# Kernel optimization log

Hardware: AMD Instinct MI355X
Metric: run time of the kernel (lower is better)

The kernel has to match this reference:

```python
import jax, jax.numpy as jnp
import numpy as np

N, C, H, W = 4, 256, 64, 64
K, G, PAD, STRIDE, DIL = 3, 8, 1, 1, 1
GC = C // G      # channels per group
P = K * K        # sampling points per group
HIN, WIN = H + 2 * PAD, W + 2 * PAD
BN_EPS = 1e-5
LN_EPS = 1e-5


def setup_inputs():
    key = jax.random.key(0)
    ks = jax.random.split(key, 8)
    f32 = jnp.float32
    return {
        "x": jax.random.normal(ks[0], (N, C, H, W), dtype=f32),
        "w_in": jax.random.normal(ks[1], (C, C), dtype=f32) * 0.05,
        "b_in": jnp.zeros((C,), f32),
        "w_dw": jax.random.normal(ks[2], (C, 1, K, K), dtype=f32) * 0.1,
        "b_dw": jnp.zeros((C,), f32),
        "ln_g": jnp.ones((C,), f32), "ln_b": jnp.zeros((C,), f32),
        "w_off": jax.random.normal(ks[3], (C, G * P * 2), dtype=f32) * 0.01,
        "b_off": jax.random.normal(ks[4], (G * P * 2,), dtype=f32) * 0.01,
        "w_mask": jax.random.normal(ks[5], (C, G * P), dtype=f32) * 0.01,
        "b_mask": jnp.zeros((G * P,), f32),
        "w_out": jax.random.normal(ks[6], (C, C), dtype=f32) * 0.05,
        "b_out": jnp.zeros((C,), f32),
        "bn_g": jnp.ones((C,), f32), "bn_b": jnp.zeros((C,), f32),
        "bn_mean": jnp.zeros((C,), f32), "bn_var": jnp.ones((C,), f32),
    }


def _bilinear(img, grid):
    # img: (B, Cc, Hh, Ww); grid: (B, S, P, 2) normalized to [-1,1],
    # matches F.grid_sample(mode='bilinear', padding_mode='zeros', align_corners=False)
    B, Cc, Hh, Ww = img.shape
    gx = (grid[..., 0] + 1.0) * 0.5 * Ww - 0.5
    gy = (grid[..., 1] + 1.0) * 0.5 * Hh - 0.5
    x0 = jnp.floor(gx)
    y0 = jnp.floor(gy)
    wx = gx - x0
    wy = gy - y0
    flat = img.reshape(B, Cc, Hh * Ww)

    def tap(xi, yi, wgt):
        valid = (xi >= 0) & (xi <= Ww - 1) & (yi >= 0) & (yi <= Hh - 1)
        idx = (jnp.clip(yi, 0, Hh - 1) * Ww + jnp.clip(xi, 0, Ww - 1)).astype(jnp.int32)
        v = jax.vmap(lambda im, ix: im[:, ix])(flat, idx)   # (B, Cc, S, P)
        return v * (wgt * valid.astype(img.dtype))[:, None]

    return (tap(x0, y0, (1 - wx) * (1 - wy)) + tap(x0 + 1, y0, wx * (1 - wy))
            + tap(x0, y0 + 1, (1 - wx) * wy) + tap(x0 + 1, y0 + 1, wx * wy))


def _forward(x, w_in, b_in, w_dw, b_dw, ln_g, ln_b, w_off, b_off,
             w_mask, b_mask, w_out, b_out, bn_g, bn_b, bn_mean, bn_var):
    xl = jnp.transpose(x, (0, 2, 3, 1))                      # (N,H,W,C) channels-last
    x_proj = xl @ w_in + b_in                                # input_proj
    # depthwise conv + LayerNorm + GELU feature branch for offset/mask prediction
    dw = jax.lax.conv_general_dilated(
        x, w_dw, (1, 1), ((PAD, PAD), (PAD, PAD)),
        feature_group_count=C, dimension_numbers=("NCHW", "OIHW", "NCHW"))
    dw = jnp.transpose(dw + b_dw[None, :, None, None], (0, 2, 3, 1))
    mu = dw.mean(-1, keepdims=True)
    var = ((dw - mu) ** 2).mean(-1, keepdims=True)
    dw = (dw - mu) * jax.lax.rsqrt(var + LN_EPS) * ln_g + ln_b
    x1 = jax.nn.gelu(dw, approximate=False)
    offset = x1 @ w_off + b_off                              # (N,H,W,G*P*2)
    mask = jax.nn.softmax((x1 @ w_mask + b_mask).reshape(N, H, W, G, P), axis=-1)
    # reference points + dilation kernel grid, normalized to padded input, (x,y) order
    ry = ((DIL * (K - 1)) // 2 + 0.5 + jnp.arange(H, dtype=x.dtype) * STRIDE) / HIN
    rx = ((DIL * (K - 1)) // 2 + 0.5 + jnp.arange(W, dtype=x.dtype) * STRIDE) / WIN
    ref = jnp.stack(jnp.broadcast_arrays(rx[None, :], ry[:, None]), axis=-1)  # (H,W,2)
    px = (jnp.arange(K, dtype=x.dtype) * DIL - (DIL * (K - 1)) // 2) / WIN
    py = (jnp.arange(K, dtype=x.dtype) * DIL - (DIL * (K - 1)) // 2) / HIN
    gx, gy = jnp.meshgrid(px, py, indexing="ij")             # kw-major flattening as in DCNv3
    kgrid = jnp.stack([gx, gy], -1).reshape(P, 2)
    norm = jnp.array([WIN, HIN], dtype=x.dtype)
    loc = (ref[None, :, :, None, None, :] + kgrid[None, None, None, None, :, :]
           + offset.reshape(N, H, W, G, P, 2) / norm)        # (N,H,W,G,P,2), offset_scale=1
    sgrid = 2.0 * loc - 1.0
    # group-split padded value tensor and deformable sampling
    xp = jnp.pad(x_proj, ((0, 0), (PAD, PAD), (PAD, PAD), (0, 0)))
    img = jnp.transpose(xp, (0, 3, 1, 2)).reshape(N * G, GC, HIN, WIN)
    sg = jnp.transpose(sgrid.reshape(N, H * W, G, P, 2), (0, 2, 1, 3, 4)).reshape(N * G, H * W, P, 2)
    sampled = _bilinear(img, sg)                             # (N*G, GC, H*W, P)
    m = jnp.transpose(mask.reshape(N, H * W, G, P), (0, 2, 1, 3)).reshape(N * G, 1, H * W, P)
    agg = (sampled * m).sum(-1)                              # (N*G, GC, H*W)
    y = jnp.transpose(agg.reshape(N, C, H * W), (0, 2, 1)).reshape(N, H, W, C)
    y = y @ w_out + b_out                                    # output_proj
    y = jnp.transpose(y, (0, 3, 1, 2))                       # back to NCHW
    y = (y - bn_mean[None, :, None, None]) * jax.lax.rsqrt(bn_var + BN_EPS)[None, :, None, None]
    y = y * bn_g[None, :, None, None] + bn_b[None, :, None, None]
    return y * jax.nn.sigmoid(y)                             # SiLU (Conv.default_act)


def reference(x, w_in, b_in, w_dw, b_dw, ln_g, ln_b, w_off, b_off,
              w_mask, b_mask, w_out, b_out, bn_g, bn_b, bn_mean, bn_var):
    return _forward(x, w_in, b_in, w_dw, b_dw, ln_g, ln_b, w_off, b_off,
                    w_mask, b_mask, w_out, b_out, bn_g, bn_b, bn_mean, bn_var)
```

## Files before the change

### kernel.cpp

```cpp
#include <hip/hip_runtime.h>
#include <math.h>

#define NB   4
#define CCH  256
#define HH   64
#define WW   64
#define GG   8
#define GCH  32
#define PP   9
#define HIN  66
#define WIN  66
#define HWSZ 4096
#define NPIX 16384

#define XP_ELEMS  (NB*HIN*WIN*CCH)
#define X1_ELEMS  (NPIX*CCH)
#define AGG_ELEMS (NPIX*CCH)
#define OFF_ELEMS (NPIX*144)
#define MSK_ELEMS (NPIX*72)

typedef __attribute__((ext_vector_type(8))) short bf16x8;
typedef __attribute__((ext_vector_type(4))) float f32x4;

__device__ __forceinline__ unsigned short f2bf(float f) {
    unsigned int u = __float_as_uint(f);
    unsigned int r = (u + 0x7FFFu + ((u >> 16) & 1u)) >> 16;
    return (unsigned short)r;
}
__device__ __forceinline__ float bf2f(unsigned short s) {
    return __uint_as_float(((unsigned int)s) << 16);
}
__device__ __forceinline__ unsigned int f2bf_pk(float lo, float hi) {
    return (unsigned int)f2bf(lo) | ((unsigned int)f2bf(hi) << 16);
}

#define AK 40

__global__ __launch_bounds__(64) void k_zero_ring(unsigned short* __restrict__ xp)
{
    int b = blockIdx.x;
    int n = b / 260;
    int rp = b % 260;
    int h, w;
    if (rp < 66)       { h = 0;        w = rp; }
    else if (rp < 132) { h = 65;       w = rp - 66; }
    else if (rp < 196) { h = rp - 131; w = 0; }
    else               { h = rp - 195; w = 65; }
    uint2 z = make_uint2(0u, 0u);
    *(uint2*)&xp[(((size_t)n * HIN + h) * WIN + w) * CCH + threadIdx.x * 4] = z;
}

__global__ __launch_bounds__(256) void k_gemm_in(
    const float* __restrict__ x, const float* __restrict__ w_in,
    const float* __restrict__ b_in, unsigned short* __restrict__ xp)
{
    __shared__ short As[128 * AK];
    __shared__ short Ws[64 * AK];

    const int m0  = blockIdx.x * 128;
    const int co0 = blockIdx.y * 64;
    const int tid = threadIdx.x;
    const int n   = m0 >> 12;
    const int hw0 = m0 & 4095;

    const int wave = tid >> 6;
    const int lane = tid & 63;
    const int r16  = lane & 15;
    const int quad = lane >> 4;
    const int mw   = wave * 32;

    const float* xa = x + (size_t)n * CCH * HWSZ + hw0;

    f32x4 acc[2][4];
#pragma unroll
    for (int i = 0; i < 2; i++)
#pragma unroll
        for (int j = 0; j < 4; j++) acc[i][j] = (f32x4){0.f, 0.f, 0.f, 0.f};

    for (int k0 = 0; k0 < CCH; k0 += 32) {
#pragma unroll
        for (int l = 0; l < 8; l++) {
            int idx = tid + l * 256;
            int m = idx & 127, kp = idx >> 7;
            float v0 = xa[(size_t)(k0 + 2 * kp) * HWSZ + m];
            float v1 = xa[(size_t)(k0 + 2 * kp + 1) * HWSZ + m];
            ((unsigned int*)As)[(m * AK) / 2 + kp] = f2bf_pk(v0, v1);
        }
#pragma unroll
        for (int l = 0; l < 4; l++) {
            int idx = tid + l * 256;
            int nn = idx & 63, kp = idx >> 6;
            float v0 = w_in[(size_t)(k0 + 2 * kp) * CCH + co0 + nn];
            float v1 = w_in[(size_t)(k0 + 2 * kp + 1) * CCH + co0 + nn];
            ((unsigned int*)Ws)[(nn * AK) / 2 + kp] = f2bf_pk(v0, v1);
        }
        __syncthreads();

        bf16x8 a0 = *(const bf16x8*)&As[(mw + r16) * AK + quad * 8];
        bf16x8 a1 = *(const bf16x8*)&As[(mw + 16 + r16) * AK + quad * 8];
#pragma unroll
        for (int nt = 0; nt < 4; nt++) {
            bf16x8 bfr = *(const bf16x8*)&Ws[(nt * 16 + r16) * AK + quad * 8];
            acc[0][nt] = __builtin_amdgcn_mfma_f32_16x16x32_bf16(a0, bfr, acc[0][nt], 0, 0, 0);
            acc[1][nt] = __builtin_amdgcn_mfma_f32_16x16x32_bf16(a1, bfr, acc[1][nt], 0, 0, 0);
        }
        __syncthreads();
    }

#pragma unroll
    for (int nt = 0; nt < 4; nt++) {
        int co = co0 + nt * 16 + r16;
        float bias = b_in[co];
#pragma unroll
        for (int mt = 0; mt < 2; mt++) {
            int mbase = mw + mt * 16 + quad * 4;
#pragma unroll
            for (int r = 0; r < 4; r++) {
                int hw = hw0 + mbase + r;
                int h = hw >> 6, w = hw & 63;
                xp[(((size_t)n * HIN + (h + 1)) * WIN + (w + 1)) * CCH + co] =
                    f2bf(acc[mt][nt][r] + bias);
            }
        }
    }
}

#define SDW_STRIDE 258
__global__ __launch_bounds__(512) void k_dw_ln_gelu(
    const float* __restrict__ x, const float* __restrict__ w_dw,
    const float* __restrict__ b_dw, const float* __restrict__ ln_g,
    const float* __restrict__ ln_b, unsigned short* __restrict__ x1)
{
    __shared__ unsigned short sdw[64 * SDW_STRIDE];
    __shared__ float r1s[8][64];
    __shared__ float r2s[8][64];
    __shared__ float mu_s[64];
    __shared__ float rs_s[64];

    const int h = blockIdx.x;
    const int n = blockIdx.y;
    const int tid = threadIdx.x;
    const int wave = tid >> 6;
    const int lane = tid & 63;

    const float* xn = x + (size_t)n * CCH * HWSZ;
    const bool h0ok = (h > 0);
    const bool h2ok = (h < HH - 1);

    float s1 = 0.f, s2 = 0.f;

#pragma unroll 4
    for (int it = 0; it < 32; it++) {
        const int c = it * 8 + wave;
        const float* xc = xn + (size_t)c * HWSZ + h * WW + lane;
        float v0 = h0ok ? xc[-WW] : 0.f;
        float v1 = xc[0];
        float v2 = h2ok ? xc[WW] : 0.f;

        const float* wk = w_dw + c * 9;
        float acc = b_dw[c];

        float l0 = __shfl_up(v0, 1);  if (lane == 0)  l0 = 0.f;
        float r0 = __shfl_down(v0, 1); if (lane == 63) r0 = 0.f;
        acc += wk[0] * l0 + wk[1] * v0 + wk[2] * r0;

        float l1 = __shfl_up(v1, 1);  if (lane == 0)  l1 = 0.f;
        float r1 = __shfl_down(v1, 1); if (lane == 63) r1 = 0.f;
        acc += wk[3] * l1 + wk[4] * v1 + wk[5] * r1;

        float l2 = __shfl_up(v2, 1);  if (lane == 0)  l2 = 0.f;
        float r2 = __shfl_down(v2, 1); if (lane == 63) r2 = 0.f;
        acc += wk[6] * l2 + wk[7] * v2 + wk[8] * r2;

        s1 += acc;
        s2 += acc * acc;
        sdw[lane * SDW_STRIDE + c] = f2bf(acc);
    }

    r1s[wave][lane] = s1;
    r2s[wave][lane] = s2;
    __syncthreads();

    if (tid < 64) {
        float a1 = 0.f, a2 = 0.f;
#pragma unroll
        for (int q = 0; q < 8; q++) { a1 += r1s[q][tid]; a2 += r2s[q][tid]; }
        float mu = a1 * (1.0f / 256.0f);
        float var = a2 * (1.0f / 256.0f) - mu * mu;
        mu_s[tid] = mu;
        rs_s[tid] = rsqrtf(var + 1e-5f);
    }
    __syncthreads();

    const int c0 = (tid & 63) * 4;
    const int wq = tid >> 6;
    float g4[4], b4[4];
#pragma unroll
    for (int i = 0; i < 4; i++) { g4[i] = ln_g[c0 + i]; b4[i] = ln_b[c0 + i]; }

    unsigned short* x1p = x1 + (((size_t)n * HH + h) * WW) * CCH + c0;
#pragma unroll
    for (int pass = 0; pass < 8; pass++) {
        int w = wq + pass * 8;
        float mu = mu_s[w], rs = rs_s[w];
        const unsigned short* row = &sdw[w * SDW_STRIDE + c0];
        unsigned short tmp[4];
#pragma unroll
        for (int i = 0; i < 4; i++) {
            float v = (bf2f(row[i]) - mu) * rs * g4[i] + b4[i];
            tmp[i] = f2bf(0.5f * v * (1.0f + erff(v * 0.70710678118654752f)));
        }
        ushort4 o; o.x = tmp[0]; o.y = tmp[1]; o.z = tmp[2]; o.w = tmp[3];
        *(ushort4*)&x1p[(size_t)w * CCH] = o;
    }
}

__global__ __launch_bounds__(256) void k_gemm_offmask(
    const unsigned short* __restrict__ x1, const float* __restrict__ w_off,
    const float* __restrict__ b_off, const float* __restrict__ w_mask,
    const float* __restrict__ b_mask, float* __restrict__ off,
    float* __restrict__ msk)
{
    __shared__ short As[128 * AK];
    __shared__ short Ws[64 * AK];

    const int m0  = blockIdx.x * 128;
    const int co0 = blockIdx.y * 64;
    const int tid = threadIdx.x;

    const int wave = tid >> 6;
    const int lane = tid & 63;
    const int r16  = lane & 15;
    const int quad = lane >> 4;
    const int mw   = wave * 32;

    f32x4 acc[2][4];
#pragma unroll
    for (int i = 0; i < 2; i++)
#pragma unroll
        for (int j = 0; j < 4; j++) acc[i][j] = (f32x4){0.f, 0.f, 0.f, 0.f};

    for (int k0 = 0; k0 < CCH; k0 += 32) {
#pragma unroll
        for (int l = 0; l < 2; l++) {
            int idx = tid + l * 256;
            int m = idx >> 2, kq = idx & 3;
            uint4 v = *(const uint4*)&x1[(size_t)(m0 + m) * CCH + k0 + kq * 8];
            *(uint4*)&As[m * AK + kq * 8] = v;
        }
#pragma unroll
        for (int l = 0; l < 4; l++) {
            int idx = tid + l * 256;
            int nn = idx & 63, kp = idx >> 6;
            int col = co0 + nn;
            float v0 = 0.f, v1 = 0.f;
            if (col < 144) {
                v0 = w_off[(size_t)(k0 + 2 * kp) * 144 + col];
                v1 = w_off[(size_t)(k0 + 2 * kp + 1) * 144 + col];
            } else if (col < 216) {
                v0 = w_mask[(size_t)(k0 + 2 * kp) * 72 + col - 144];
                v1 = w_mask[(size_t)(k0 + 2 * kp + 1) * 72 + col - 144];
            }
            ((unsigned int*)Ws)[(nn * AK) / 2 + kp] = f2bf_pk(v0, v1);
        }
        __syncthreads();

        bf16x8 a0 = *(const bf16x8*)&As[(mw + r16) * AK + quad * 8];
        bf16x8 a1 = *(const bf16x8*)&As[(mw + 16 + r16) * AK + quad * 8];
#pragma unroll
        for (int nt = 0; nt < 4; nt++) {
            bf16x8 bfr = *(const bf16x8*)&Ws[(nt * 16 + r16) * AK + quad * 8];
            acc[0][nt] = __builtin_amdgcn_mfma_f32_16x16x32_bf16(a0, bfr, acc[0][nt], 0, 0, 0);
            acc[1][nt] = __builtin_amdgcn_mfma_f32_16x16x32_bf16(a1, bfr, acc[1][nt], 0, 0, 0);
        }
        __syncthreads();
    }

#pragma unroll
    for (int nt = 0; nt < 4; nt++) {
        int col = co0 + nt * 16 + r16;
        if (col >= 216) continue;
        float bias = (col < 144) ? b_off[col] : b_mask[col - 144];
#pragma unroll
        for (int mt = 0; mt < 2; mt++) {
            int mbase = m0 + mw + mt * 16 + quad * 4;
#pragma unroll
            for (int r = 0; r < 4; r++) {
                int p = mbase + r;
                float v = acc[mt][nt][r] + bias;
                if (col < 144) off[(size_t)p * 144 + col] = v;
                else           msk[(size_t)p * 72 + col - 144] = v;
            }
        }
    }
}

__global__ __launch_bounds__(256) void k_sample_agg(
    const unsigned short* __restrict__ xp, const float* __restrict__ off,
    const float* __restrict__ msk, unsigned short* __restrict__ agg)
{
    __shared__ float  sm[288];
    __shared__ int2   tco[288];
    __shared__ float4 twt[288];

    const int tid = threadIdx.x;
    const int s0 = blockIdx.x * 4;

    if (tid < 32) {
        const int pix = tid >> 3, g = tid & 7;
        const float* mskp = msk + (size_t)(s0 + pix) * 72 + g * 9;
        float e[9];
        float mx = -1e30f;
#pragma unroll
        for (int p = 0; p < PP; p++) { e[p] = mskp[p]; mx = fmaxf(mx, e[p]); }
        float sum = 0.f;
#pragma unroll
        for (int p = 0; p < PP; p++) { e[p] = __expf(e[p] - mx); sum += e[p]; }
        float rs = 1.0f / sum;
#pragma unroll
        for (int p = 0; p < PP; p++) sm[tid * 9 + p] = e[p] * rs;
    }
    __syncthreads();

    for (int idx = tid; idx < 288; idx += 256) {
        int pix = idx / 72;
        int rem = idx - pix * 72;
        int g = rem / 9;
        int p = rem - g * 9;
        int s = s0 + pix;
        int hw = s & 4095;
        int h = hw >> 6, w = hw & 63;
        const float* offp = off + (size_t)s * 144 + g * 18 + p * 2;
        float ox = offp[0], oy = offp[1];
        int i = p / 3, j = p - i * 3;
        float fx = (float)(w + i) + ox;
        float fy = (float)(h + j) + oy;
        float x0f = floorf(fx), y0f = floorf(fy);
        int x0 = (int)x0f, y0 = (int)y0f;
        float wx = fx - x0f, wy = fy - y0f;
        float m = sm[idx];
        float w00 = (1.f - wx) * (1.f - wy) * m;
        float w10 = wx * (1.f - wy) * m;
        float w01 = (1.f - wx) * wy * m;
        float w11 = wx * wy * m;
        int x1c = x0 + 1, y1c = y0 + 1;
        if (!((x0  >= 0) && (x0  < WIN))) { w00 = 0.f; w01 = 0.f; }
        if (!((x1c >= 0) && (x1c < WIN))) { w10 = 0.f; w11 = 0.f; }
        if (!((y0  >= 0) && (y0  < HIN))) { w00 = 0.f; w10 = 0.f; }
        if (!((y1c >= 0) && (y1c < HIN))) { w01 = 0.f; w11 = 0.f; }
        int cx0 = min(max(x0, 0), WIN - 1), cx1 = min(max(x1c, 0), WIN - 1);
        int cy0 = min(max(y0, 0), HIN - 1), cy1 = min(max(y1c, 0), HIN - 1);
        tco[idx] = make_int2(cx0 | (cx1 << 16), cy0 | (cy1 << 16));
        twt[idx] = make_float4(w00, w10, w01, w11);
    }
    __syncthreads();

    const int pix = tid >> 6;
    const int lane = tid & 63;
    const int g = lane >> 3, c4 = lane & 7;
    const int s = s0 + pix;
    const int n = s >> 12;
    const unsigned short* base = xp + (size_t)n * HIN * WIN * CCH + g * GCH + c4 * 4;
    const int tbase = pix * 72 + g * 9;

    float ax = 0.f, ay = 0.f, az = 0.f, aw = 0.f;
#pragma unroll
    for (int p = 0; p < PP; p++) {
        int2 cc = tco[tbase + p];
        float4 wt = twt[tbase + p];
        int cx0 = cc.x & 0xFFFF, cx1 = cc.x >> 16;
        int cy0 = cc.y & 0xFFFF, cy1 = cc.y >> 16;
        const unsigned short* r0 = base + (size_t)(cy0 * WIN) * CCH;
        const unsigned short* r1 = base + (size_t)(cy1 * WIN) * CCH;
        ushort4 v00 = *(const ushort4*)&r0[(size_t)cx0 * CCH];
        ushort4 v10 = *(const ushort4*)&r0[(size_t)cx1 * CCH];
        ushort4 v01 = *(const ushort4*)&r1[(size_t)cx0 * CCH];
        ushort4 v11 = *(const ushort4*)&r1[(size_t)cx1 * CCH];
        ax += wt.x * bf2f(v00.x) + wt.y * bf2f(v10.x) + wt.z * bf2f(v01.x) + wt.w * bf2f(v11.x);
        ay += wt.x * bf2f(v00.y) + wt.y * bf2f(v10.y) + wt.z * bf2f(v01.y) + wt.w * bf2f(v11.y);
        az += wt.x * bf2f(v00.z) + wt.y * bf2f(v10.z) + wt.z * bf2f(v01.z) + wt.w * bf2f(v11.z);
        aw += wt.x * bf2f(v00.w) + wt.y * bf2f(v10.w) + wt.z * bf2f(v01.w) + wt.w * bf2f(v11.w);
    }

    ushort4 o; o.x = f2bf(ax); o.y = f2bf(ay); o.z = f2bf(az); o.w = f2bf(aw);
    *(ushort4*)&agg[(size_t)s * CCH + g * GCH + c4 * 4] = o;
}

__global__ __launch_bounds__(256) void k_gemm_out(
    const unsigned short* __restrict__ agg, const float* __restrict__ w_out,
    const float* __restrict__ b_out, const float* __restrict__ bn_g,
    const float* __restrict__ bn_b, const float* __restrict__ bn_mean,
    const float* __restrict__ bn_var, float* __restrict__ out)
{
    __shared__ short As[128 * AK];
    __shared__ short Ws[64 * AK];

    const int m0  = blockIdx.x * 128;
    const int co0 = blockIdx.y * 64;
    const int tid = threadIdx.x;
    const int n   = m0 >> 12;
    const int hw0 = m0 & 4095;

    const int wave = tid >> 6;
    const int lane = tid & 63;
    const int r16  = lane & 15;
    const int quad = lane >> 4;
    const int mw   = wave * 32;

    f32x4 acc[2][4];
#pragma unroll
    for (int i = 0; i < 2; i++)
#pragma unroll
        for (int j = 0; j < 4; j++) acc[i][j] = (f32x4){0.f, 0.f, 0.f, 0.f};

    for (int k0 = 0; k0 < CCH; k0 += 32) {
#pragma unroll
        for (int l = 0; l < 2; l++) {
            int idx = tid + l * 256;
            int m = idx >> 2, kq = idx & 3;
            uint4 v = *(const uint4*)&agg[(size_t)(m0 + m) * CCH + k0 + kq * 8];
            *(uint4*)&As[m * AK + kq * 8] = v;
        }
#pragma unroll
        for (int l = 0; l < 4; l++) {
            int idx = tid + l * 256;
            int nn = idx & 63, kp = idx >> 6;
            float v0 = w_out[(size_t)(k0 + 2 * kp) * CCH + co0 + nn];
            float v1 = w_out[(size_t)(k0 + 2 * kp + 1) * CCH + co0 + nn];
            ((unsigned int*)Ws)[(nn * AK) / 2 + kp] = f2bf_pk(v0, v1);
        }
        __syncthreads();

        bf16x8 a0 = *(const bf16x8*)&As[(mw + r16) * AK + quad * 8];
        bf16x8 a1 = *(const bf16x8*)&As[(mw + 16 + r16) * AK + quad * 8];
#pragma unroll
        for (int nt = 0; nt < 4; nt++) {
            bf16x8 bfr = *(const bf16x8*)&Ws[(nt * 16 + r16) * AK + quad * 8];
            acc[0][nt] = __builtin_amdgcn_mfma_f32_16x16x32_bf16(a0, bfr, acc[0][nt], 0, 0, 0);
            acc[1][nt] = __builtin_amdgcn_mfma_f32_16x16x32_bf16(a1, bfr, acc[1][nt], 0, 0, 0);
        }
        __syncthreads();
    }

#pragma unroll
    for (int nt = 0; nt < 4; nt++) {
        int co = co0 + nt * 16 + r16;
        float mean = bn_mean[co];
        float rstd = rsqrtf(bn_var[co] + 1e-5f);
        float gg = bn_g[co], bb = bn_b[co], bo = b_out[co];
#pragma unroll
        for (int mt = 0; mt < 2; mt++) {
            int hwb = hw0 + mw + mt * 16 + quad * 4;
            float tmp[4];
#pragma unroll
            for (int r = 0; r < 4; r++) {
                float y = acc[mt][nt][r] + bo;
                float yh = (y - mean) * rstd * gg + bb;
                tmp[r] = yh / (1.0f + __expf(-yh));
            }
            float4 v = make_float4(tmp[0], tmp[1], tmp[2], tmp[3]);
            *(float4*)&out[((size_t)n * CCH + co) * HWSZ + hwb] = v;
        }
    }
}

extern "C" void kernel_launch(void* const* d_in, const int* in_sizes, int n_in,
                              void* d_out, int out_size, void* d_ws, size_t ws_size,
                              hipStream_t stream)
{
    const float* x       = (const float*)d_in[0];
    const float* w_in    = (const float*)d_in[1];
    const float* b_in    = (const float*)d_in[2];
    const float* w_dw    = (const float*)d_in[3];
    const float* b_dw    = (const float*)d_in[4];
    const float* ln_g    = (const float*)d_in[5];
    const float* ln_b    = (const float*)d_in[6];
    const float* w_off   = (const float*)d_in[7];
    const float* b_off   = (const float*)d_in[8];
    const float* w_mask  = (const float*)d_in[9];
    const float* b_mask  = (const float*)d_in[10];
    const float* w_out   = (const float*)d_in[11];
    const float* b_out   = (const float*)d_in[12];
    const float* bn_g    = (const float*)d_in[13];
    const float* bn_b    = (const float*)d_in[14];
    const float* bn_mean = (const float*)d_in[15];
    const float* bn_var  = (const float*)d_in[16];
    float* out = (float*)d_out;

    unsigned short* xp  = (unsigned short*)d_ws;
    unsigned short* x1  = xp + XP_ELEMS;
    unsigned short* agg = x1 + X1_ELEMS;
    float* off = (float*)(agg + AGG_ELEMS);
    float* msk = off + OFF_ELEMS;

    k_zero_ring<<<dim3(1040), 64, 0, stream>>>(xp);
    k_gemm_in<<<dim3(128, 4), 256, 0, stream>>>(x, w_in, b_in, xp);
    k_dw_ln_gelu<<<dim3(64, 4), 512, 0, stream>>>(x, w_dw, b_dw, ln_g, ln_b, x1);
    k_gemm_offmask<<<dim3(128, 4), 256, 0, stream>>>(x1, w_off, b_off, w_mask, b_mask, off, msk);
    k_sample_agg<<<dim3(4096), 256, 0, stream>>>(xp, off, msk, agg);
    k_gemm_out<<<dim3(128, 4), 256, 0, stream>>>(agg, w_out, b_out, bn_g, bn_b, bn_mean, bn_var, out);
}
```

Baseline: 181.5 us.

## Pre-convert input and weights to bf16 once; widen sampling loads to 8 channels

```diff
diff --git a/kernel.cpp b/kernel.cpp
--- a/kernel.cpp
+++ b/kernel.cpp
@@ -13,9 +13,13 @@
 #define HWSZ 4096
 #define NPIX 16384
 
+#define X16_ELEMS (NPIX*CCH)
 #define XP_ELEMS  (NB*HIN*WIN*CCH)
 #define X1_ELEMS  (NPIX*CCH)
 #define AGG_ELEMS (NPIX*CCH)
+#define WIN16_ELEMS (CCH*CCH)
+#define WOUT16_ELEMS (CCH*CCH)
+#define WOM16_ELEMS (CCH*216)
 #define OFF_ELEMS (NPIX*144)
 #define MSK_ELEMS (NPIX*72)
 
@@ -30,28 +34,58 @@
 __device__ __forceinline__ float bf2f(unsigned short s) {
     return __uint_as_float(((unsigned int)s) << 16);
 }
-__device__ __forceinline__ unsigned int f2bf_pk(float lo, float hi) {
-    return (unsigned int)f2bf(lo) | ((unsigned int)f2bf(hi) << 16);
-}
 
 #define AK 40
 
-__global__ __launch_bounds__(64) void k_zero_ring(unsigned short* __restrict__ xp)
-{
-    int b = blockIdx.x;
-    int n = b / 260;
-    int rp = b % 260;
-    int h, w;
-    if (rp < 66)       { h = 0;        w = rp; }
-    else if (rp < 132) { h = 65;       w = rp - 66; }
-    else if (rp < 196) { h = rp - 131; w = 0; }
-    else               { h = rp - 195; w = 65; }
-    uint2 z = make_uint2(0u, 0u);
-    *(uint2*)&xp[(((size_t)n * HIN + h) * WIN + w) * CCH + threadIdx.x * 4] = z;
+__global__ __launch_bounds__(256) void k_prep(
+    const float* __restrict__ x, const float* __restrict__ w_in,
+    const float* __restrict__ w_off, const float* __restrict__ w_mask,
+    const float* __restrict__ w_out, unsigned short* __restrict__ x16,
+    unsigned short* __restrict__ w_in16, unsigned short* __restrict__ wom16,
+    unsigned short* __restrict__ w_out16, unsigned short* __restrict__ xp)
+{
+    const int b = blockIdx.x;
+    const int tid = threadIdx.x;
+    if (b < 2048) {
+        size_t i0 = (size_t)b * 2048 + tid * 4;
+#pragma unroll
+        for (int h = 0; h < 2; h++) {
+            float4 v = *(const float4*)&x[i0 + h * 1024];
+            ushort4 o;
+            o.x = f2bf(v.x); o.y = f2bf(v.y); o.z = f2bf(v.z); o.w = f2bf(v.w);
+            *(ushort4*)&x16[i0 + h * 1024] = o;
+        }
+    } else if (b < 2096) {
+        int gtid = (b - 2048) * 256 + tid;
+        for (int i = gtid; i < 186368; i += 12288) {
+            if (i < 65536) {
+                w_in16[i] = f2bf(w_in[i]);
+            } else if (i < 131072) {
+                int j = i - 65536;
+                w_out16[j] = f2bf(w_out[j]);
+            } else {
+                int j = i - 131072;
+                int r = j / 216, c = j - r * 216;
+                float v = (c < 144) ? w_off[r * 144 + c] : w_mask[r * 72 + c - 144];
+                wom16[j] = f2bf(v);
+            }
+        }
+    } else {
+        int idx = (b - 2096) * 256 + tid;
+        int seg = idx >> 6, ln = idx & 63;
+        int n = seg / 260, rp = seg % 260;
+        int h, w;
+        if (rp < 66)       { h = 0;        w = rp; }
+        else if (rp < 132) { h = 65;       w = rp - 66; }
+        else if (rp < 196) { h = rp - 131; w = 0; }
+        else               { h = rp - 195; w = 65; }
+        uint2 z = make_uint2(0u, 0u);
+        *(uint2*)&xp[(((size_t)n * HIN + h) * WIN + w) * CCH + ln * 4] = z;
+    }
 }
 
 __global__ __launch_bounds__(256) void k_gemm_in(
-    const float* __restrict__ x, const float* __restrict__ w_in,
+    const unsigned short* __restrict__ x16, const unsigned short* __restrict__ w16,
     const float* __restrict__ b_in, unsigned short* __restrict__ xp)
 {
     __shared__ short As[128 * AK];
@@ -69,7 +103,7 @@
     const int quad = lane >> 4;
     const int mw   = wave * 32;
 
-    const float* xa = x + (size_t)n * CCH * HWSZ + hw0;
+    const unsigned short* xa = x16 + (size_t)n * CCH * HWSZ + hw0;
 
     f32x4 acc[2][4];
 #pragma unroll
@@ -78,21 +112,27 @@
         for (int j = 0; j < 4; j++) acc[i][j] = (f32x4){0.f, 0.f, 0.f, 0.f};
 
     for (int k0 = 0; k0 < CCH; k0 += 32) {
-#pragma unroll
-        for (int l = 0; l < 8; l++) {
-            int idx = tid + l * 256;
-            int m = idx & 127, kp = idx >> 7;
-            float v0 = xa[(size_t)(k0 + 2 * kp) * HWSZ + m];
-            float v1 = xa[(size_t)(k0 + 2 * kp + 1) * HWSZ + m];
-            ((unsigned int*)As)[(m * AK) / 2 + kp] = f2bf_pk(v0, v1);
-        }
 #pragma unroll
         for (int l = 0; l < 4; l++) {
             int idx = tid + l * 256;
-            int nn = idx & 63, kp = idx >> 6;
-            float v0 = w_in[(size_t)(k0 + 2 * kp) * CCH + co0 + nn];
-            float v1 = w_in[(size_t)(k0 + 2 * kp + 1) * CCH + co0 + nn];
-            ((unsigned int*)Ws)[(nn * AK) / 2 + kp] = f2bf_pk(v0, v1);
+            int m = idx & 127, kph = idx >> 7;
+            unsigned int u0 = xa[(size_t)(k0 + 4 * kph + 0) * HWSZ + m];
+            unsigned int u1 = xa[(size_t)(k0 + 4 * kph + 1) * HWSZ + m];
+            unsigned int u2 = xa[(size_t)(k0 + 4 * kph + 2) * HWSZ + m];
+            unsigned int u3 = xa[(size_t)(k0 + 4 * kph + 3) * HWSZ + m];
+            uint2 pk = make_uint2(u0 | (u1 << 16), u2 | (u3 << 16));
+            *(uint2*)&As[m * AK + kph * 4] = pk;
+        }
+#pragma unroll
+        for (int l = 0; l < 2; l++) {
+            int idx = tid + l * 256;
+            int nn = idx & 63, kph = idx >> 6;
+            unsigned int u0 = w16[(size_t)(k0 + 4 * kph + 0) * CCH + co0 + nn];
+            unsigned int u1 = w16[(size_t)(k0 + 4 * kph + 1) * CCH + co0 + nn];
+            unsigned int u2 = w16[(size_t)(k0 + 4 * kph + 2) * CCH + co0 + nn];
+            unsigned int u3 = w16[(size_t)(k0 + 4 * kph + 3) * CCH + co0 + nn];
+            uint2 pk = make_uint2(u0 | (u1 << 16), u2 | (u3 << 16));
+            *(uint2*)&Ws[nn * AK + kph * 4] = pk;
         }
         __syncthreads();
 
@@ -127,7 +167,7 @@
 
 #define SDW_STRIDE 258
 __global__ __launch_bounds__(512) void k_dw_ln_gelu(
-    const float* __restrict__ x, const float* __restrict__ w_dw,
+    const unsigned short* __restrict__ x16, const float* __restrict__ w_dw,
     const float* __restrict__ b_dw, const float* __restrict__ ln_g,
     const float* __restrict__ ln_b, unsigned short* __restrict__ x1)
 {
@@ -143,7 +183,7 @@
     const int wave = tid >> 6;
     const int lane = tid & 63;
 
-    const float* xn = x + (size_t)n * CCH * HWSZ;
+    const unsigned short* xn = x16 + (size_t)n * CCH * HWSZ;
     const bool h0ok = (h > 0);
     const bool h2ok = (h < HH - 1);
 
@@ -152,10 +192,10 @@
 #pragma unroll 4
     for (int it = 0; it < 32; it++) {
         const int c = it * 8 + wave;
-        const float* xc = xn + (size_t)c * HWSZ + h * WW + lane;
-        float v0 = h0ok ? xc[-WW] : 0.f;
-        float v1 = xc[0];
-        float v2 = h2ok ? xc[WW] : 0.f;
+        const unsigned short* xc = xn + (size_t)c * HWSZ + h * WW + lane;
+        float v0 = h0ok ? bf2f(xc[-WW]) : 0.f;
+        float v1 = bf2f(xc[0]);
+        float v2 = h2ok ? bf2f(xc[WW]) : 0.f;
 
         const float* wk = w_dw + c * 9;
         float acc = b_dw[c];
@@ -216,10 +256,9 @@
 }
 
 __global__ __launch_bounds__(256) void k_gemm_offmask(
-    const unsigned short* __restrict__ x1, const float* __restrict__ w_off,
-    const float* __restrict__ b_off, const float* __restrict__ w_mask,
-    const float* __restrict__ b_mask, float* __restrict__ off,
-    float* __restrict__ msk)
+    const unsigned short* __restrict__ x1, const unsigned short* __restrict__ wom16,
+    const float* __restrict__ b_off, const float* __restrict__ b_mask,
+    float* __restrict__ off, float* __restrict__ msk)
 {
     __shared__ short As[128 * AK];
     __shared__ short Ws[64 * AK];
@@ -249,19 +288,19 @@
             *(uint4*)&As[m * AK + kq * 8] = v;
         }
 #pragma unroll
-        for (int l = 0; l < 4; l++) {
+        for (int l = 0; l < 2; l++) {
             int idx = tid + l * 256;
-            int nn = idx & 63, kp = idx >> 6;
+            int nn = idx & 63, kph = idx >> 6;
             int col = co0 + nn;
-            float v0 = 0.f, v1 = 0.f;
-            if (col < 144) {
-                v0 = w_off[(size_t)(k0 + 2 * kp) * 144 + col];
-                v1 = w_off[(size_t)(k0 + 2 * kp + 1) * 144 + col];
-            } else if (col < 216) {
-                v0 = w_mask[(size_t)(k0 + 2 * kp) * 72 + col - 144];
-                v1 = w_mask[(size_t)(k0 + 2 * kp + 1) * 72 + col - 144];
+            unsigned int u0 = 0, u1 = 0, u2 = 0, u3 = 0;
+            if (col < 216) {
+                u0 = wom16[(size_t)(k0 + 4 * kph + 0) * 216 + col];
+                u1 = wom16[(size_t)(k0 + 4 * kph + 1) * 216 + col];
+                u2 = wom16[(size_t)(k0 + 4 * kph + 2) * 216 + col];
+                u3 = wom16[(size_t)(k0 + 4 * kph + 3) * 216 + col];
             }
-            ((unsigned int*)Ws)[(nn * AK) / 2 + kp] = f2bf_pk(v0, v1);
+            uint2 pk = make_uint2(u0 | (u1 << 16), u2 | (u3 << 16));
+            *(uint2*)&Ws[nn * AK + kph * 4] = pk;
         }
         __syncthreads();
 
@@ -295,18 +334,29 @@
     }
 }
 
+__device__ __forceinline__ void acc8_tap(float* a, uint4 vv, float wgt) {
+    a[0] += wgt * __uint_as_float(vv.x << 16);
+    a[1] += wgt * __uint_as_float(vv.x & 0xffff0000u);
+    a[2] += wgt * __uint_as_float(vv.y << 16);
+    a[3] += wgt * __uint_as_float(vv.y & 0xffff0000u);
+    a[4] += wgt * __uint_as_float(vv.z << 16);
+    a[5] += wgt * __uint_as_float(vv.z & 0xffff0000u);
+    a[6] += wgt * __uint_as_float(vv.w << 16);
+    a[7] += wgt * __uint_as_float(vv.w & 0xffff0000u);
+}
+
 __global__ __launch_bounds__(256) void k_sample_agg(
     const unsigned short* __restrict__ xp, const float* __restrict__ off,
     const float* __restrict__ msk, unsigned short* __restrict__ agg)
 {
-    __shared__ float  sm[288];
-    __shared__ int2   tco[288];
-    __shared__ float4 twt[288];
+    __shared__ float  sm[576];
+    __shared__ int2   tco[576];
+    __shared__ float4 twt[576];
 
     const int tid = threadIdx.x;
-    const int s0 = blockIdx.x * 4;
-
-    if (tid < 32) {
+    const int s0 = blockIdx.x * 8;
+
+    if (tid < 64) {
         const int pix = tid >> 3, g = tid & 7;
         const float* mskp = msk + (size_t)(s0 + pix) * 72 + g * 9;
         float e[9];
@@ -322,7 +372,7 @@
     }
     __syncthreads();
 
-    for (int idx = tid; idx < 288; idx += 256) {
+    for (int idx = tid; idx < 576; idx += 256) {
         int pix = idx / 72;
         int rem = idx - pix * 72;
         int g = rem / 9;
@@ -355,15 +405,18 @@
     }
     __syncthreads();
 
-    const int pix = tid >> 6;
-    const int lane = tid & 63;
-    const int g = lane >> 3, c4 = lane & 7;
+    const int pix = tid >> 5;
+    const int l5 = tid & 31;
+    const int g = l5 >> 2, c8 = l5 & 3;
     const int s = s0 + pix;
     const int n = s >> 12;
-    const unsigned short* base = xp + (size_t)n * HIN * WIN * CCH + g * GCH + c4 * 4;
+    const unsigned short* base = xp + (size_t)n * HIN * WIN * CCH + g * GCH + c8 * 8;
     const int tbase = pix * 72 + g * 9;
 
-    float ax = 0.f, ay = 0.f, az = 0.f, aw = 0.f;
+    float a[8];
+#pragma unroll
+    for (int i = 0; i < 8; i++) a[i] = 0.f;
+
 #pragma unroll
     for (int p = 0; p < PP; p++) {
         int2 cc = tco[tbase + p];
@@ -372,22 +425,26 @@
         int cy0 = cc.y & 0xFFFF, cy1 = cc.y >> 16;
         const unsigned short* r0 = base + (size_t)(cy0 * WIN) * CCH;
         const unsigned short* r1 = base + (size_t)(cy1 * WIN) * CCH;
-        ushort4 v00 = *(const ushort4*)&r0[(size_t)cx0 * CCH];
-        ushort4 v10 = *(const ushort4*)&r0[(size_t)cx1 * CCH];
-        ushort4 v01 = *(const ushort4*)&r1[(size_t)cx0 * CCH];
-        ushort4 v11 = *(const ushort4*)&r1[(size_t)cx1 * CCH];
-        ax += wt.x * bf2f(v00.x) + wt.y * bf2f(v10.x) + wt.z * bf2f(v01.x) + wt.w * bf2f(v11.x);
-        ay += wt.x * bf2f(v00.y) + wt.y * bf2f(v10.y) + wt.z * bf2f(v01.y) + wt.w * bf2f(v11.y);
-        az += wt.x * bf2f(v00.z) + wt.y * bf2f(v10.z) + wt.z * bf2f(v01.z) + wt.w * bf2f(v11.z);
-        aw += wt.x * bf2f(v00.w) + wt.y * bf2f(v10.w) + wt.z * bf2f(v01.w) + wt.w * bf2f(v11.w);
-    }
-
-    ushort4 o; o.x = f2bf(ax); o.y = f2bf(ay); o.z = f2bf(az); o.w = f2bf(aw);
-    *(ushort4*)&agg[(size_t)s * CCH + g * GCH + c4 * 4] = o;
+        uint4 v00 = *(const uint4*)&r0[(size_t)cx0 * CCH];
+        uint4 v10 = *(const uint4*)&r0[(size_t)cx1 * CCH];
+        uint4 v01 = *(const uint4*)&r1[(size_t)cx0 * CCH];
+        uint4 v11 = *(const uint4*)&r1[(size_t)cx1 * CCH];
+        acc8_tap(a, v00, wt.x);
+        acc8_tap(a, v10, wt.y);
+        acc8_tap(a, v01, wt.z);
+        acc8_tap(a, v11, wt.w);
+    }
+
+    uint4 o;
+    o.x = (unsigned int)f2bf(a[0]) | ((unsigned int)f2bf(a[1]) << 16);
+    o.y = (unsigned int)f2bf(a[2]) | ((unsigned int)f2bf(a[3]) << 16);
+    o.z = (unsigned int)f2bf(a[4]) | ((unsigned int)f2bf(a[5]) << 16);
+    o.w = (unsigned int)f2bf(a[6]) | ((unsigned int)f2bf(a[7]) << 16);
+    *(uint4*)&agg[(size_t)s * CCH + g * GCH + c8 * 8] = o;
 }
 
 __global__ __launch_bounds__(256) void k_gemm_out(
-    const unsigned short* __restrict__ agg, const float* __restrict__ w_out,
+    const unsigned short* __restrict__ agg, const unsigned short* __restrict__ w16,
     const float* __restrict__ b_out, const float* __restrict__ bn_g,
     const float* __restrict__ bn_b, const float* __restrict__ bn_mean,
     const float* __restrict__ bn_var, float* __restrict__ out)
@@ -422,12 +479,15 @@
             *(uint4*)&As[m * AK + kq * 8] = v;
         }
 #pragma unroll
-        for (int l = 0; l < 4; l++) {
+        for (int l = 0; l < 2; l++) {
             int idx = tid + l * 256;
-            int nn = idx & 63, kp = idx >> 6;
-            float v0 = w_out[(size_t)(k0 + 2 * kp) * CCH + co0 + nn];
-            float v1 = w_out[(size_t)(k0 + 2 * kp + 1) * CCH + co0 + nn];
-            ((unsigned int*)Ws)[(nn * AK) / 2 + kp] = f2bf_pk(v0, v1);
+            int nn = idx & 63, kph = idx >> 6;
+            unsigned int u0 = w16[(size_t)(k0 + 4 * kph + 0) * CCH + co0 + nn];
+            unsigned int u1 = w16[(size_t)(k0 + 4 * kph + 1) * CCH + co0 + nn];
+            unsigned int u2 = w16[(size_t)(k0 + 4 * kph + 2) * CCH + co0 + nn];
+            unsigned int u3 = w16[(size_t)(k0 + 4 * kph + 3) * CCH + co0 + nn];
+            uint2 pk = make_uint2(u0 | (u1 << 16), u2 | (u3 << 16));
+            *(uint2*)&Ws[nn * AK + kph * 4] = pk;
         }
         __syncthreads();
 
@@ -487,16 +547,21 @@
     const float* bn_var  = (const float*)d_in[16];
     float* out = (float*)d_out;
 
-    unsigned short* xp  = (unsigned short*)d_ws;
-    unsigned short* x1  = xp + XP_ELEMS;
-    unsigned short* agg = x1 + X1_ELEMS;
-    float* off = (float*)(agg + AGG_ELEMS);
+    unsigned short* x16    = (unsigned short*)d_ws;
+    unsigned short* xp     = x16 + X16_ELEMS;
+    unsigned short* x1     = xp + XP_ELEMS;
+    unsigned short* agg    = x1 + X1_ELEMS;
+    unsigned short* w_in16 = agg + AGG_ELEMS;
+    unsigned short* w_out16= w_in16 + WIN16_ELEMS;
+    unsigned short* wom16  = w_out16 + WOUT16_ELEMS;
+    float* off = (float*)(wom16 + WOM16_ELEMS);
     float* msk = off + OFF_ELEMS;
 
-    k_zero_ring<<<dim3(1040), 64, 0, stream>>>(xp);
-    k_gemm_in<<<dim3(128, 4), 256, 0, stream>>>(x, w_in, b_in, xp);
-    k_dw_ln_gelu<<<dim3(64, 4), 512, 0, stream>>>(x, w_dw, b_dw, ln_g, ln_b, x1);
-    k_gemm_offmask<<<dim3(128, 4), 256, 0, stream>>>(x1, w_off, b_off, w_mask, b_mask, off, msk);
-    k_sample_agg<<<dim3(4096), 256, 0, stream>>>(xp, off, msk, agg);
-    k_gemm_out<<<dim3(128, 4), 256, 0, stream>>>(agg, w_out, b_out, bn_g, bn_b, bn_mean, bn_var, out);
-}
+    k_prep<<<dim3(2356), 256, 0, stream>>>(x, w_in, w_off, w_mask, w_out,
+                                           x16, w_in16, wom16, w_out16, xp);
+    k_gemm_in<<<dim3(128, 4), 256, 0, stream>>>(x16, w_in16, b_in, xp);
+    k_dw_ln_gelu<<<dim3(64, 4), 512, 0, stream>>>(x16, w_dw, b_dw, ln_g, ln_b, x1);
+    k_gemm_offmask<<<dim3(128, 4), 256, 0, stream>>>(x1, wom16, b_off, b_mask, off, msk);
+    k_sample_agg<<<dim3(2048), 256, 0, stream>>>(xp, off, msk, agg);
+    k_gemm_out<<<dim3(128, 4), 256, 0, stream>>>(agg, w_out16, b_out, bn_g, bn_b, bn_mean, bn_var, out);
+}
```

Measured after the change: 198.6 us. 1.09x slower.

## Register-prefetch next K tile in GEMMs and widen sampling loads to 8 channels

Applied to the files above, without the earlier changes.

```diff
diff --git a/kernel.cpp b/kernel.cpp
--- a/kernel.cpp
+++ b/kernel.cpp
@@ -77,24 +77,56 @@
 #pragma unroll
         for (int j = 0; j < 4; j++) acc[i][j] = (f32x4){0.f, 0.f, 0.f, 0.f};
 
+    float apre[16];
+    float wpre[8];
+
+#pragma unroll
+    for (int l = 0; l < 8; l++) {
+        int idx = tid + l * 256;
+        int m = idx & 127, kp = idx >> 7;
+        apre[2 * l + 0] = xa[(size_t)(2 * kp) * HWSZ + m];
+        apre[2 * l + 1] = xa[(size_t)(2 * kp + 1) * HWSZ + m];
+    }
+#pragma unroll
+    for (int l = 0; l < 4; l++) {
+        int idx = tid + l * 256;
+        int nn = idx & 63, kp = idx >> 6;
+        wpre[2 * l + 0] = w_in[(size_t)(2 * kp) * CCH + co0 + nn];
+        wpre[2 * l + 1] = w_in[(size_t)(2 * kp + 1) * CCH + co0 + nn];
+    }
+
     for (int k0 = 0; k0 < CCH; k0 += 32) {
 #pragma unroll
         for (int l = 0; l < 8; l++) {
             int idx = tid + l * 256;
             int m = idx & 127, kp = idx >> 7;
-            float v0 = xa[(size_t)(k0 + 2 * kp) * HWSZ + m];
-            float v1 = xa[(size_t)(k0 + 2 * kp + 1) * HWSZ + m];
-            ((unsigned int*)As)[(m * AK) / 2 + kp] = f2bf_pk(v0, v1);
+            ((unsigned int*)As)[(m * AK) / 2 + kp] = f2bf_pk(apre[2 * l], apre[2 * l + 1]);
         }
 #pragma unroll
         for (int l = 0; l < 4; l++) {
             int idx = tid + l * 256;
             int nn = idx & 63, kp = idx >> 6;
-            float v0 = w_in[(size_t)(k0 + 2 * kp) * CCH + co0 + nn];
-            float v1 = w_in[(size_t)(k0 + 2 * kp + 1) * CCH + co0 + nn];
-            ((unsigned int*)Ws)[(nn * AK) / 2 + kp] = f2bf_pk(v0, v1);
+            ((unsigned int*)Ws)[(nn * AK) / 2 + kp] = f2bf_pk(wpre[2 * l], wpre[2 * l + 1]);
         }
         __syncthreads();
+
+        if (k0 + 32 < CCH) {
+            int k1 = k0 + 32;
+#pragma unroll
+            for (int l = 0; l < 8; l++) {
+                int idx = tid + l * 256;
+                int m = idx & 127, kp = idx >> 7;
+                apre[2 * l + 0] = xa[(size_t)(k1 + 2 * kp) * HWSZ + m];
+                apre[2 * l + 1] = xa[(size_t)(k1 + 2 * kp + 1) * HWSZ + m];
+            }
+#pragma unroll
+            for (int l = 0; l < 4; l++) {
+                int idx = tid + l * 256;
+                int nn = idx & 63, kp = idx >> 6;
+                wpre[2 * l + 0] = w_in[(size_t)(k1 + 2 * kp) * CCH + co0 + nn];
+                wpre[2 * l + 1] = w_in[(size_t)(k1 + 2 * kp + 1) * CCH + co0 + nn];
+            }
+        }
 
         bf16x8 a0 = *(const bf16x8*)&As[(mw + r16) * AK + quad * 8];
         bf16x8 a1 = *(const bf16x8*)&As[(mw + 16 + r16) * AK + quad * 8];
@@ -234,36 +266,73 @@
     const int quad = lane >> 4;
     const int mw   = wave * 32;
 
+    const int am = tid >> 2, akq = tid & 3;
+    const int wn = tid & 63, wkp = tid >> 6;
+
     f32x4 acc[2][4];
 #pragma unroll
     for (int i = 0; i < 2; i++)
 #pragma unroll
         for (int j = 0; j < 4; j++) acc[i][j] = (f32x4){0.f, 0.f, 0.f, 0.f};
 
+    uint4 apre[2];
+    float wpre[8];
+
+#pragma unroll
+    for (int l = 0; l < 2; l++) {
+        int m = am + l * 64;
+        apre[l] = *(const uint4*)&x1[(size_t)(m0 + m) * CCH + akq * 8];
+    }
+#pragma unroll
+    for (int l = 0; l < 4; l++) {
+        int kp = wkp + l * 4;
+        int col = co0 + wn;
+        float v0 = 0.f, v1 = 0.f;
+        if (col < 144) {
+            v0 = w_off[(size_t)(2 * kp) * 144 + col];
+            v1 = w_off[(size_t)(2 * kp + 1) * 144 + col];
+        } else if (col < 216) {
+            v0 = w_mask[(size_t)(2 * kp) * 72 + col - 144];
+            v1 = w_mask[(size_t)(2 * kp + 1) * 72 + col - 144];
+        }
+        wpre[2 * l] = v0; wpre[2 * l + 1] = v1;
+    }
+
     for (int k0 = 0; k0 < CCH; k0 += 32) {
 #pragma unroll
         for (int l = 0; l < 2; l++) {
-            int idx = tid + l * 256;
-            int m = idx >> 2, kq = idx & 3;
-            uint4 v = *(const uint4*)&x1[(size_t)(m0 + m) * CCH + k0 + kq * 8];
-            *(uint4*)&As[m * AK + kq * 8] = v;
+            int m = am + l * 64;
+            *(uint4*)&As[m * AK + akq * 8] = apre[l];
         }
 #pragma unroll
         for (int l = 0; l < 4; l++) {
-            int idx = tid + l * 256;
-            int nn = idx & 63, kp = idx >> 6;
-            int col = co0 + nn;
-            float v0 = 0.f, v1 = 0.f;
-            if (col < 144) {
-                v0 = w_off[(size_t)(k0 + 2 * kp) * 144 + col];
-                v1 = w_off[(size_t)(k0 + 2 * kp + 1) * 144 + col];
-            } else if (col < 216) {
-                v0 = w_mask[(size_t)(k0 + 2 * kp) * 72 + col - 144];
-                v1 = w_mask[(size_t)(k0 + 2 * kp + 1) * 72 + col - 144];
-            }
-            ((unsigned int*)Ws)[(nn * AK) / 2 + kp] = f2bf_pk(v0, v1);
+            int kp = wkp + l * 4;
+            ((unsigned int*)Ws)[(wn * AK) / 2 + kp] = f2bf_pk(wpre[2 * l], wpre[2 * l + 1]);
         }
         __syncthreads();
+
+        if (k0 + 32 < CCH) {
+            int k1 = k0 + 32;
+#pragma unroll
+            for (int l = 0; l < 2; l++) {
+                int m = am + l * 64;
+                apre[l] = *(const uint4*)&x1[(size_t)(m0 + m) * CCH + k1 + akq * 8];
+            }
+#pragma unroll
+            for (int l = 0; l < 4; l++) {
+                int kp = wkp + l * 4;
+                int col = co0 + wn;
+                float v0 = 0.f, v1 = 0.f;
+                if (col < 144) {
+                    v0 = w_off[(size_t)(k1 + 2 * kp) * 144 + col];
+                    v1 = w_off[(size_t)(k1 + 2 * kp + 1) * 144 + col];
+                } else if (col < 216) {
+                    v0 = w_mask[(size_t)(k1 + 2 * kp) * 72 + col - 144];
+                    v1 = w_mask[(size_t)(k1 + 2 * kp + 1) * 72 + col - 144];
+                }
+                wpre[2 * l] = v0; wpre[2 * l + 1] = v1;
+            }
+        }
 
         bf16x8 a0 = *(const bf16x8*)&As[(mw + r16) * AK + quad * 8];
         bf16x8 a1 = *(const bf16x8*)&As[(mw + 16 + r16) * AK + quad * 8];
@@ -295,18 +364,29 @@
     }
 }
 
+__device__ __forceinline__ void acc8_tap(float* a, uint4 vv, float wgt) {
+    a[0] += wgt * __uint_as_float(vv.x << 16);
+    a[1] += wgt * __uint_as_float(vv.x & 0xffff0000u);
+    a[2] += wgt * __uint_as_float(vv.y << 16);
+    a[3] += wgt * __uint_as_float(vv.y & 0xffff0000u);
+    a[4] += wgt * __uint_as_float(vv.z << 16);
+    a[5] += wgt * __uint_as_float(vv.z & 0xffff0000u);
+    a[6] += wgt * __uint_as_float(vv.w << 16);
+    a[7] += wgt * __uint_as_float(vv.w & 0xffff0000u);
+}
+
 __global__ __launch_bounds__(256) void k_sample_agg(
     const unsigned short* __restrict__ xp, const float* __restrict__ off,
     const float* __restrict__ msk, unsigned short* __restrict__ agg)
 {
-    __shared__ float  sm[288];
-    __shared__ int2   tco[288];
-    __shared__ float4 twt[288];
+    __shared__ float  sm[576];
+    __shared__ int2   tco[576];
+    __shared__ float4 twt[576];
 
     const int tid = threadIdx.x;
-    const int s0 = blockIdx.x * 4;
-
-    if (tid < 32) {
+    const int s0 = blockIdx.x * 8;
+
+    if (tid < 64) {
         const int pix = tid >> 3, g = tid & 7;
         const float* mskp = msk + (size_t)(s0 + pix) * 72 + g * 9;
         float e[9];
@@ -322,7 +402,7 @@
     }
     __syncthreads();
 
-    for (int idx = tid; idx < 288; idx += 256) {
+    for (int idx = tid; idx < 576; idx += 256) {
         int pix = idx / 72;
         int rem = idx - pix * 72;
         int g = rem / 9;
@@ -355,15 +435,18 @@
     }
     __syncthreads();
 
-    const int pix = tid >> 6;
-    const int lane = tid & 63;
-    const int g = lane >> 3, c4 = lane & 7;
+    const int pix = tid >> 5;
+    const int l5 = tid & 31;
+    const int g = l5 >> 2, c8 = l5 & 3;
     const int s = s0 + pix;
     const int n = s >> 12;
-    const unsigned short* base = xp + (size_t)n * HIN * WIN * CCH + g * GCH + c4 * 4;
+    const unsigned short* base = xp + (size_t)n * HIN * WIN * CCH + g * GCH + c8 * 8;
     const int tbase = pix * 72 + g * 9;
 
-    float ax = 0.f, ay = 0.f, az = 0.f, aw = 0.f;
+    float a[8];
+#pragma unroll
+    for (int i = 0; i < 8; i++) a[i] = 0.f;
+
 #pragma unroll
     for (int p = 0; p < PP; p++) {
         int2 cc = tco[tbase + p];
@@ -372,18 +455,22 @@
         int cy0 = cc.y & 0xFFFF, cy1 = cc.y >> 16;
         const unsigned short* r0 = base + (size_t)(cy0 * WIN) * CCH;
         const unsigned short* r1 = base + (size_t)(cy1 * WIN) * CCH;
-        ushort4 v00 = *(const ushort4*)&r0[(size_t)cx0 * CCH];
-        ushort4 v10 = *(const ushort4*)&r0[(size_t)cx1 * CCH];
-        ushort4 v01 = *(const ushort4*)&r1[(size_t)cx0 * CCH];
-        ushort4 v11 = *(const ushort4*)&r1[(size_t)cx1 * CCH];
-        ax += wt.x * bf2f(v00.x) + wt.y * bf2f(v10.x) + wt.z * bf2f(v01.x) + wt.w * bf2f(v11.x);
-        ay += wt.x * bf2f(v00.y) + wt.y * bf2f(v10.y) + wt.z * bf2f(v01.y) + wt.w * bf2f(v11.y);
-        az += wt.x * bf2f(v00.z) + wt.y * bf2f(v10.z) + wt.z * bf2f(v01.z) + wt.w * bf2f(v11.z);
-        aw += wt.x * bf2f(v00.w) + wt.y * bf2f(v10.w) + wt.z * bf2f(v01.w) + wt.w * bf2f(v11.w);
-    }
-
-    ushort4 o; o.x = f2bf(ax); o.y = f2bf(ay); o.z = f2bf(az); o.w = f2bf(aw);
-    *(ushort4*)&agg[(size_t)s * CCH + g * GCH + c4 * 4] = o;
+        uint4 v00 = *(const uint4*)&r0[(size_t)cx0 * CCH];
+        uint4 v10 = *(const uint4*)&r0[(size_t)cx1 * CCH];
+        uint4 v01 = *(const uint4*)&r1[(size_t)cx0 * CCH];
+        uint4 v11 = *(const uint4*)&r1[(size_t)cx1 * CCH];
+        acc8_tap(a, v00, wt.x);
+        acc8_tap(a, v10, wt.y);
+        acc8_tap(a, v01, wt.z);
+        acc8_tap(a, v11, wt.w);
+    }
+
+    uint4 o;
+    o.x = (unsigned int)f2bf(a[0]) | ((unsigned int)f2bf(a[1]) << 16);
+    o.y = (unsigned int)f2bf(a[2]) | ((unsigned int)f2bf(a[3]) << 16);
+    o.z = (unsigned int)f2bf(a[4]) | ((unsigned int)f2bf(a[5]) << 16);
+    o.w = (unsigned int)f2bf(a[6]) | ((unsigned int)f2bf(a[7]) << 16);
+    *(uint4*)&agg[(size_t)s * CCH + g * GCH + c8 * 8] = o;
 }
 
 __global__ __launch_bounds__(256) void k_gemm_out(
@@ -407,29 +494,57 @@
     const int quad = lane >> 4;
     const int mw   = wave * 32;
 
+    const int am = tid >> 2, akq = tid & 3;
+    const int wn = tid & 63, wkp = tid >> 6;
+
     f32x4 acc[2][4];
 #pragma unroll
     for (int i = 0; i < 2; i++)
 #pragma unroll
         for (int j = 0; j < 4; j++) acc[i][j] = (f32x4){0.f, 0.f, 0.f, 0.f};
 
+    uint4 apre[2];
+    float wpre[8];
+
+#pragma unroll
+    for (int l = 0; l < 2; l++) {
+        int m = am + l * 64;
+        apre[l] = *(const uint4*)&agg[(size_t)(m0 + m) * CCH + akq * 8];
+    }
+#pragma unroll
+    for (int l = 0; l < 4; l++) {
+        int kp = wkp + l * 4;
+        wpre[2 * l + 0] = w_out[(size_t)(2 * kp) * CCH + co0 + wn];
+        wpre[2 * l + 1] = w_out[(size_t)(2 * kp + 1) * CCH + co0 + wn];
+    }
+
     for (int k0 = 0; k0 < CCH; k0 += 32) {
 #pragma unroll
         for (int l = 0; l < 2; l++) {
-            int idx = tid + l * 256;
-            int m = idx >> 2, kq = idx & 3;
-            uint4 v = *(const uint4*)&agg[(size_t)(m0 + m) * CCH + k0 + kq * 8];
-            *(uint4*)&As[m * AK + kq * 8] = v;
+            int m = am + l * 64;
+            *(uint4*)&As[m * AK + akq * 8] = apre[l];
         }
 #pragma unroll
         for (int l = 0; l < 4; l++) {
-            int idx = tid + l * 256;
-            int nn = idx & 63, kp = idx >> 6;
-            float v0 = w_out[(size_t)(k0 + 2 * kp) * CCH + co0 + nn];
-            float v1 = w_out[(size_t)(k0 + 2 * kp + 1) * CCH + co0 + nn];
-            ((unsigned int*)Ws)[(nn * AK) / 2 + kp] = f2bf_pk(v0, v1);
+            int kp = wkp + l * 4;
+            ((unsigned int*)Ws)[(wn * AK) / 2 + kp] = f2bf_pk(wpre[2 * l], wpre[2 * l + 1]);
         }
         __syncthreads();
+
+        if (k0 + 32 < CCH) {
+            int k1 = k0 + 32;
+#pragma unroll
+            for (int l = 0; l < 2; l++) {
+                int m = am + l * 64;
+                apre[l] = *(const uint4*)&agg[(size_t)(m0 + m) * CCH + k1 + akq * 8];
+            }
+#pragma unroll
+            for (int l = 0; l < 4; l++) {
+                int kp = wkp + l * 4;
+                wpre[2 * l + 0] = w_out[(size_t)(k1 + 2 * kp) * CCH + co0 + wn];
+                wpre[2 * l + 1] = w_out[(size_t)(k1 + 2 * kp + 1) * CCH + co0 + wn];
+            }
+        }
 
         bf16x8 a0 = *(const bf16x8*)&As[(mw + r16) * AK + quad * 8];
         bf16x8 a1 = *(const bf16x8*)&As[(mw + 16 + r16) * AK + quad * 8];
@@ -497,6 +612,6 @@
     k_gemm_in<<<dim3(128, 4), 256, 0, stream>>>(x, w_in, b_in, xp);
     k_dw_ln_gelu<<<dim3(64, 4), 512, 0, stream>>>(x, w_dw, b_dw, ln_g, ln_b, x1);
     k_gemm_offmask<<<dim3(128, 4), 256, 0, stream>>>(x1, w_off, b_off, w_mask, b_mask, off, msk);
-    k_sample_agg<<<dim3(4096), 256, 0, stream>>>(xp, off, msk, agg);
+    k_sample_agg<<<dim3(2048), 256, 0, stream>>>(xp, off, msk, agg);
     k_gemm_out<<<dim3(128, 4), 256, 0, stream>>>(agg, w_out, b_out, bn_g, bn_b, bn_mean, bn_var, out);
 }
```

After: 181.4 us. About the same (-0.1%).
